# Performance work log

Hardware: AMD Instinct MI355X
Metric: run time of the kernel (lower is better)

The kernel has to match this reference:

```python
import jax, jax.numpy as jnp
import numpy as np

B = 128      # batch
U = 64       # num_users (H dim)
A = 64       # num_aps   (W dim)
FIN = 1      # input_feature_dim
FPHI = 32    # phi_feature_dim
FGAM = 32    # gamma_feature_dim
PHI_OUT = 2 * FPHI   # 64
GAM_OUT = 2 * FGAM   # 64


def setup_inputs() -> dict:
    key = jax.random.key(0)
    ks = iter(jax.random.split(key, 64))

    def w(shape, scale=0.05):
        return jax.random.normal(next(ks), shape, dtype=jnp.float32) * scale

    inp = {"channel_gains": jax.random.normal(next(ks), (B, FIN, U, A), dtype=jnp.float32)}
    # Phi1: conv1 (2*FIN -> 2*FPHI), conv2 (2*FPHI -> PHI_OUT)
    inp["phi1_W1"] = w((2 * FPHI, 2 * FIN)); inp["phi1_b1"] = w((2 * FPHI,))
    inp["phi1_W2"] = w((PHI_OUT, 2 * FPHI)); inp["phi1_b2"] = w((PHI_OUT,))
    # Phi2-5 (stacked): conv1 (GAM_OUT+FIN -> 2*FPHI), conv2 (2*FPHI -> PHI_OUT)
    inp["phiK_W1"] = w((4, 2 * FPHI, GAM_OUT + FIN)); inp["phiK_b1"] = w((4, 2 * FPHI))
    inp["phiK_W2"] = w((4, PHI_OUT, 2 * FPHI)); inp["phiK_b2"] = w((4, PHI_OUT))
    # Gamma1: conv1 (FIN+PHI_OUT -> 2*FGAM), conv2 (2*FGAM -> GAM_OUT)
    inp["gamma1_W1"] = w((2 * FGAM, FIN + PHI_OUT)); inp["gamma1_b1"] = w((2 * FGAM,))
    inp["gamma1_W2"] = w((GAM_OUT, 2 * FGAM)); inp["gamma1_b2"] = w((GAM_OUT,))
    # Gamma2-4 (stacked): conv1 (GAM_OUT+PHI_OUT -> 2*FGAM), conv2 (2*FGAM -> GAM_OUT)
    inp["gammaK_W1"] = w((3, 2 * FGAM, GAM_OUT + PHI_OUT)); inp["gammaK_b1"] = w((3, 2 * FGAM))
    inp["gammaK_W2"] = w((3, GAM_OUT, 2 * FGAM)); inp["gammaK_b2"] = w((3, GAM_OUT))
    # Gamma5 (final): conv1 (GAM_OUT+PHI_OUT -> 2*FGAM), conv2 (2*FGAM -> 1)
    inp["gamma5_W1"] = w((2 * FGAM, GAM_OUT + PHI_OUT)); inp["gamma5_b1"] = w((2 * FGAM,))
    inp["gamma5_W2"] = w((1, 2 * FGAM)); inp["gamma5_b2"] = w((1,))
    return inp


def conv1x1(x, W, b):
    # 1x1 conv on NCHW == per-pixel GEMM over channels
    return jnp.einsum('bcua,oc->boua', x, W) + b[None, :, None, None]


def post_users(x, f, ex_u):
    # keep first f channels; aggregate (sum-exclude-self over users) the next f
    c0 = x[:, :f]
    c1 = jnp.einsum('uv,bcva->bcua', ex_u, x[:, f:2 * f]) / (U - 1)
    return jnp.concatenate([c0, c1], axis=1)


def phi_block(x, W1, b1, W2, b2, ex_u):
    r = post_users(jax.nn.relu(conv1x1(x, W1, b1)), FPHI, ex_u)
    return post_users(conv1x1(r, W2, b2), FPHI, ex_u)


def gamma_block(x, W1, b1, W2, b2, ex_u, final):
    r = post_users(jax.nn.relu(conv1x1(x, W1, b1)), FGAM, ex_u)
    r = conv1x1(r, W2, b2)
    if not final:
        r = post_users(jax.nn.relu(r), FGAM, ex_u)
    return r


def reference(channel_gains, phi1_W1, phi1_b1, phi1_W2, phi1_b2,
              phiK_W1, phiK_b1, phiK_W2, phiK_b2,
              gamma1_W1, gamma1_b1, gamma1_W2, gamma1_b2,
              gammaK_W1, gammaK_b1, gammaK_W2, gammaK_b2,
              gamma5_W1, gamma5_b1, gamma5_W2, gamma5_b2):
    ex_u = jnp.ones((U, U), jnp.float32) - jnp.eye(U, dtype=jnp.float32)
    ex_a = jnp.ones((A, A), jnp.float32) - jnp.eye(A, dtype=jnp.float32)

    def node(msgs, feats, W1, b1, W2, b2, final):
        agg = jnp.einsum('bcuv,va->bcua', msgs, ex_a) / (A - 1)
        return gamma_block(jnp.concatenate([feats, agg], axis=1), W1, b1, W2, b2, ex_u, final)

    cg = channel_gains
    msgs = phi_block(jnp.concatenate([cg, cg], axis=1), phi1_W1, phi1_b1, phi1_W2, phi1_b2, ex_u)
    r = node(msgs, cg, gamma1_W1, gamma1_b1, gamma1_W2, gamma1_b2, False)
    for i in range(4):  # phi2..phi5 / gamma2..gamma5
        msgs = phi_block(jnp.concatenate([cg, r], axis=1),
                         phiK_W1[i], phiK_b1[i], phiK_W2[i], phiK_b2[i], ex_u)
        if i < 3:
            r = node(msgs, r, gammaK_W1[i], gammaK_b1[i], gammaK_W2[i], gammaK_b2[i], False)
        else:
            r = node(msgs, r, gamma5_W1, gamma5_b1, gamma5_W2, gamma5_b2, True)
    return r
```

## Files before the change

kernel.cpp:

```cpp
#include <hip/hip_runtime.h>


typedef __attribute__((ext_vector_type(8))) short bf16x8;
typedef __attribute__((ext_vector_type(4))) float f32x4;
typedef unsigned int u32;
typedef unsigned short u16;

__device__ __forceinline__ u32 bf16_rne(float x) {
    u32 u = __float_as_uint(x);
    return (u + 0x7fffu + ((u >> 16) & 1u)) >> 16;
}
__device__ __forceinline__ float bflo(u32 w) { return __uint_as_float(w << 16); }
__device__ __forceinline__ float bfhi(u32 w) { return __uint_as_float(w & 0xffff0000u); }

__device__ __forceinline__ u32 cvt2(float a, float b) {
    u32 w;
    asm("v_cvt_pk_bf16_f32 %0, %1, %2" : "=v"(w) : "v"(a), "v"(b));
    return w;
}

template <int CTRL>
__device__ __forceinline__ float dpp_mov(float v) {
    int x = __builtin_amdgcn_update_dpp(0, __float_as_int(v), CTRL, 0xF, 0xF, true);
    return __int_as_float(x);
}
__device__ __forceinline__ float row16_sum(float s) {
    s += dpp_mov<0xB1>(s);
    s += dpp_mov<0x4E>(s);
    s += dpp_mov<0x141>(s);
    s += dpp_mov<0x140>(s);
    return s;
}

__global__ __launch_bounds__(256) void prep_kernel(
    const float* __restrict__ cg, float* __restrict__ cgT,
    u16* __restrict__ packs, float* __restrict__ w0s,
    const float* __restrict__ phi1_W1, const float* __restrict__ phi1_W2,
    const float* __restrict__ phiK_W1, const float* __restrict__ phiK_W2,
    const float* __restrict__ g1_W1,   const float* __restrict__ g1_W2,
    const float* __restrict__ gK_W1,   const float* __restrict__ gK_W2,
    const float* __restrict__ g5_W1)
{
    const int bid = blockIdx.x;
    const int t = threadIdx.x;
    if (bid < 352) {
        int tid = bid * 256 + t;
        int layer, rem, nch;
        if (tid < 57344) { layer = tid >> 12; rem = tid & 4095; nch = 2; }
        else { layer = 14 + ((tid - 57344) >> 13); rem = (tid - 57344) & 8191; nch = 4; }
        const float* src; int stride, colOff; size_t dstBase;
        switch (layer) {
            case 0:  src = phi1_W2;                      stride = 64;  colOff = 0; dstBase = 0; break;
            case 1: case 2: case 3: case 4: {
                int k = layer - 1; src = phiK_W1 + k * 4160; stride = 65; colOff = 1;
                dstBase = 8192 + (size_t)k * 8192; break; }
            case 5: case 6: case 7: case 8: {
                int k = layer - 5; src = phiK_W2 + k * 4096; stride = 64; colOff = 0;
                dstBase = 40960 + (size_t)k * 8192; break; }
            case 9:  src = g1_W1;                        stride = 65;  colOff = 1; dstBase = 73728; break;
            case 10: src = g1_W2;                        stride = 64;  colOff = 0; dstBase = 81920; break;
            case 11: case 12: case 13: {
                int k = layer - 11; src = gK_W2 + k * 4096; stride = 64; colOff = 0;
                dstBase = 139264 + (size_t)k * 8192; break; }
            case 14: case 15: case 16: {
                int k = layer - 14; src = gK_W1 + k * 8192; stride = 128; colOff = 0;
                dstBase = 90112 + (size_t)k * 16384; break; }
            default: src = g5_W1;                        stride = 128; colOff = 0; dstBase = 163840; break;
        }
        int j = rem & 7;
        int lane = (rem >> 3) & 63;
        int rc = rem >> 9;
        int rb = rc / nch;
        int ch = rc - rb * nch;
        int o = 16 * rb + (lane & 15);
        int c = colOff + ch * 32 + (lane >> 4) * 8 + j;
        float wv = src[o * stride + c];
        u32 hb = bf16_rne(wv);
        u32 lb = bf16_rne(wv - bflo(hb));
        size_t base = dstBase + (size_t)rc * 1024 + lane * 8 + j;
        packs[base] = (u16)hb;
        packs[base + 512] = (u16)lb;
    } else if (bid < 354) {
        int i = (bid - 352) * 256 + t;
        if (i < 64)       w0s[i] = phi1_W1[i * 2] + phi1_W1[i * 2 + 1];
        else if (i < 320) { int k = (i - 64) >> 6; int o = (i - 64) & 63; w0s[i] = phiK_W1[k * 4160 + o * 65]; }
        else if (i < 384) { int o = i - 320; w0s[i] = g1_W1[o * 65]; }
    } else {
        int idx = (bid - 354) * 256 + t;
        int b = idx >> 12;
        int u = idx & 63;
        cgT[idx] = cg[((b << 6) + u) * 64 + ((idx >> 6) & 63)];
    }
}

template <int NCH, bool LO>
__device__ __forceinline__ void loadA(const u16* __restrict__ A, int lane, int wv,
                                      bf16x8* __restrict__ Ah, bf16x8* __restrict__ Al) {
#pragma unroll
    for (int ch = 0; ch < NCH; ++ch) {
        const u16* p = A + ((size_t)(wv * NCH + ch) * 2) * 512 + lane * 8;
        Ah[ch] = *(const bf16x8*)p;
        if constexpr (LO) Al[ch] = *(const bf16x8*)(p + 512);
    }
}

template <int NCH, int SROW, int CB, bool LO>
__device__ __forceinline__ void mfma_frags(const bf16x8* __restrict__ Ah,
                                           const bf16x8* __restrict__ Al,
                                           const u16* Xhi,
                                           int lane, f32x4 acc[4]) {
    const int n16 = lane & 15, q4 = lane >> 4;
#pragma unroll
    for (int ch = 0; ch < NCH; ++ch) {
#pragma unroll
        for (int tt = 0; tt < 4; ++tt) {
            int boff = (16 * tt + n16) * SROW + CB + ch * 32 + q4 * 8;
            bf16x8 Bh = *(const bf16x8*)(Xhi + boff);
            acc[tt] = __builtin_amdgcn_mfma_f32_16x16x32_bf16(Ah[ch], Bh, acc[tt], 0, 0, 0);
            if constexpr (LO)
                acc[tt] = __builtin_amdgcn_mfma_f32_16x16x32_bf16(Al[ch], Bh, acc[tt], 0, 0, 0);
        }
    }
}

__device__ __forceinline__ void post_users_regs(f32x4 acc[4], int wv) {
    constexpr float inv63 = 1.0f / 63.0f;
    if (wv >= 2) {
#pragma unroll
        for (int r = 0; r < 4; ++r) {
            float s = row16_sum(acc[0][r] + acc[1][r] + acc[2][r] + acc[3][r]) * inv63;
#pragma unroll
            for (int tt = 0; tt < 4; ++tt) acc[tt][r] = fmaf(acc[tt][r], -inv63, s);
        }
    }
}

template <int SROW, int CB>
__device__ __forceinline__ void stage_h(const f32x4 acc[4], u16* Xhi,
                                        int lane, int wv) {
    const int n16 = lane & 15, q4 = lane >> 4;
#pragma unroll
    for (int tt = 0; tt < 4; ++tt) {
        u32 h01 = cvt2(acc[tt][0], acc[tt][1]);
        u32 h23 = cvt2(acc[tt][2], acc[tt][3]);
        int off = (16 * tt + n16) * SROW + CB + 16 * wv + 4 * q4;
        *(uint2*)(Xhi + off) = make_uint2(h01, h23);
    }
}

template <int SROW, int CB>
__device__ __forceinline__ void stage_agg(const u32* __restrict__ ms,
                                          const float* __restrict__ Ss,
                                          u16* Xhi, int t) {
    constexpr float inv63 = 1.0f / 63.0f;
#pragma unroll
    for (int q = 0; q < 4; ++q) {
        int grp = q * 256 + t;
        int u = grp >> 4, c4 = (grp & 15) * 4;
        uint2 mw = *(const uint2*)(ms + u * 32 + (c4 >> 1));
        float4 sv = *(const float4*)(Ss + u * 64 + c4);
        float a0 = fmaf(bflo(mw.x), -inv63, sv.x);
        float a1 = fmaf(bfhi(mw.x), -inv63, sv.y);
        float a2 = fmaf(bflo(mw.y), -inv63, sv.z);
        float a3 = fmaf(bfhi(mw.y), -inv63, sv.w);
        int off = u * SROW + CB + c4;
        *(uint2*)(Xhi + off) = make_uint2(cvt2(a0, a1), cvt2(a2, a3));
    }
}

__global__ __launch_bounds__(256) void reduce_kernel(
    const u32* __restrict__ msgs, float* __restrict__ S)
{
    constexpr float inv63 = 1.0f / 63.0f;
    int idx = blockIdx.x * 256 + threadIdx.x;
    int b = idx >> 10;
    int j2 = idx & 1023;
    const u32* p = msgs + (size_t)b * 131072 + j2 * 2;
    float s0 = 0.0f, s1 = 0.0f, s2 = 0.0f, s3 = 0.0f;
#pragma unroll 8
    for (int a = 0; a < 64; ++a) {
        uint2 w = *(const uint2*)(p + (size_t)a * 2048);
        s0 += bflo(w.x);
        s1 += bfhi(w.x);
        s2 += bflo(w.y);
        s3 += bfhi(w.y);
    }
    float4 o = make_float4(s0 * inv63, s1 * inv63, s2 * inv63, s3 * inv63);
    *(float4*)(S + (size_t)b * 4096 + 4 * j2) = o;
}

__global__ __launch_bounds__(256) void phi1_kernel(
    const float* __restrict__ cgT,
    const float* __restrict__ w0, const float* __restrict__ b1,
    const u16* __restrict__ A2, const float* __restrict__ b2,
    u16* __restrict__ mOut)
{
    constexpr int SROW = 136;
    __shared__ __align__(16) u16 Xhi[64 * SROW];
    const int t = threadIdx.x;
    const u32 sb = blockIdx.x;
    const int lane = t & 63;
    const int wv = t >> 6;
    const int n16 = lane & 15, q4 = lane >> 4;

    bf16x8 A2h[2], A2l[2];
    loadA<2, false>(A2, lane, wv, A2h, A2l);

    f32x4 acc[4];
    {
        const float4 bv = *(const float4*)(b1 + 16 * wv + 4 * q4);
        const float4 w0v = *(const float4*)(w0 + 16 * wv + 4 * q4);
#pragma unroll
        for (int tt = 0; tt < 4; ++tt) {
            float cgv = cgT[(size_t)sb * 64 + 16 * tt + n16];
            acc[tt][0] = bv.x + w0v.x * cgv; acc[tt][1] = bv.y + w0v.y * cgv;
            acc[tt][2] = bv.z + w0v.z * cgv; acc[tt][3] = bv.w + w0v.w * cgv;
        }
    }
#pragma unroll
    for (int tt = 0; tt < 4; ++tt)
#pragma unroll
        for (int r = 0; r < 4; ++r) acc[tt][r] = fmaxf(acc[tt][r], 0.0f);
    post_users_regs(acc, wv);
    stage_h<SROW, 0>(acc, Xhi, lane, wv);
    __syncthreads();

    f32x4 acc2[4];
    {
        const float4 bv = *(const float4*)(b2 + 16 * wv + 4 * q4);
#pragma unroll
        for (int tt = 0; tt < 4; ++tt) { acc2[tt][0] = bv.x; acc2[tt][1] = bv.y; acc2[tt][2] = bv.z; acc2[tt][3] = bv.w; }
    }
    mfma_frags<2, SROW, 0, false>(A2h, A2l, Xhi, lane, acc2);
    post_users_regs(acc2, wv);
    stage_h<SROW, 64>(acc2, Xhi, lane, wv);
    __syncthreads();
    u16* oM = mOut + (size_t)sb * 4096;
#pragma unroll
    for (int q = 0; q < 2; ++q) {
        int grp = q * 256 + t;
        int u = grp >> 3, c8 = (grp & 7) * 8;
        *(uint4*)(oM + u * 64 + c8) = *(const uint4*)(Xhi + u * SROW + 64 + c8);
    }
}

template <int KG, bool LO>
__global__ __launch_bounds__(256) void fused_kernel(
    const float* __restrict__ cgT,
    const u16* __restrict__ rIn,
    const u32* __restrict__ mIn, const float* __restrict__ Sin,
    const u16* __restrict__ A1g, const float* __restrict__ w0g,
    const float* __restrict__ b1g,
    const u16* __restrict__ A2g, const float* __restrict__ b2g,
    const u16* __restrict__ A1p, const float* __restrict__ w0p,
    const float* __restrict__ b1p,
    const u16* __restrict__ A2p, const float* __restrict__ b2p,
    u16* __restrict__ rOut, u16* __restrict__ mOut)
{
    constexpr int SROW = (KG == 128 && LO) ? 200 : 136;
    constexpr int HB   = (SROW == 200) ? 128 : 64;
    __shared__ __align__(16) u16 Xhi[64 * SROW];
    const int t = threadIdx.x;
    const u32 sb = blockIdx.x;
    const u32 bloc = sb >> 6;
    const int lane = t & 63;
    const int wv = t >> 6;
    const int n16 = lane & 15, q4 = lane >> 4;
    constexpr int NCH1 = KG / 32;

    bf16x8 A1h[NCH1], A1l[NCH1];
    loadA<NCH1, LO>(A1g, lane, wv, A1h, A1l);

    float cgvv[4];
#pragma unroll
    for (int tt = 0; tt < 4; ++tt) cgvv[tt] = cgT[(size_t)sb * 64 + 16 * tt + n16];

    if constexpr (KG == 128) {
        const u16* rs = rIn + (size_t)sb * 4096;
#pragma unroll
        for (int q = 0; q < 2; ++q) {
            int grp = q * 256 + t;
            int u = grp >> 3, c8 = (grp & 7) * 8;
            *(uint4*)(Xhi + u * SROW + c8) = *(const uint4*)(rs + u * 64 + c8);
        }
    }
    stage_agg<SROW, KG - 64>(mIn + (size_t)sb * 2048, Sin + (size_t)bloc * 4096,
                             Xhi, t);
    __syncthreads();

    bf16x8 A2h[2], A2l[2];
    loadA<2, LO>(A2g, lane, wv, A2h, A2l);

    f32x4 acc[4];
    {
        const float4 bv = *(const float4*)(b1g + 16 * wv + 4 * q4);
#pragma unroll
        for (int tt = 0; tt < 4; ++tt) { acc[tt][0] = bv.x; acc[tt][1] = bv.y; acc[tt][2] = bv.z; acc[tt][3] = bv.w; }
    }
    if constexpr (KG == 64) {
        const float4 w0v = *(const float4*)(w0g + 16 * wv + 4 * q4);
#pragma unroll
        for (int tt = 0; tt < 4; ++tt) {
            acc[tt][0] += w0v.x * cgvv[tt]; acc[tt][1] += w0v.y * cgvv[tt];
            acc[tt][2] += w0v.z * cgvv[tt]; acc[tt][3] += w0v.w * cgvv[tt];
        }
    }
    mfma_frags<NCH1, SROW, 0, LO>(A1h, A1l, Xhi, lane, acc);
#pragma unroll
    for (int tt = 0; tt < 4; ++tt)
#pragma unroll
        for (int r = 0; r < 4; ++r) acc[tt][r] = fmaxf(acc[tt][r], 0.0f);
    post_users_regs(acc, wv);
    if constexpr (HB < KG) __syncthreads();
    stage_h<SROW, HB>(acc, Xhi, lane, wv);
    __syncthreads();

    bf16x8 A3h[2], A3l[2];
    loadA<2, LO>(A1p, lane, wv, A3h, A3l);

    f32x4 acc2[4];
    {
        const float4 bv = *(const float4*)(b2g + 16 * wv + 4 * q4);
#pragma unroll
        for (int tt = 0; tt < 4; ++tt) { acc2[tt][0] = bv.x; acc2[tt][1] = bv.y; acc2[tt][2] = bv.z; acc2[tt][3] = bv.w; }
    }
    mfma_frags<2, SROW, HB, LO>(A2h, A2l, Xhi, lane, acc2);
#pragma unroll
    for (int tt = 0; tt < 4; ++tt)
#pragma unroll
        for (int r = 0; r < 4; ++r) acc2[tt][r] = fmaxf(acc2[tt][r], 0.0f);
    post_users_regs(acc2, wv);
    stage_h<SROW, 0>(acc2, Xhi, lane, wv);
    __syncthreads();

    {
        u16* oH = rOut + (size_t)sb * 4096;
#pragma unroll
        for (int q = 0; q < 2; ++q) {
            int grp = q * 256 + t;
            int u = grp >> 3, c8 = (grp & 7) * 8;
            *(uint4*)(oH + u * 64 + c8) = *(const uint4*)(Xhi + u * SROW + c8);
        }
    }
    bf16x8 A4h[2], A4l[2];
    loadA<2, LO>(A2p, lane, wv, A4h, A4l);

    f32x4 acc3[4];
    {
        const float4 bv = *(const float4*)(b1p + 16 * wv + 4 * q4);
        const float4 w0v = *(const float4*)(w0p + 16 * wv + 4 * q4);
#pragma unroll
        for (int tt = 0; tt < 4; ++tt) {
            acc3[tt][0] = bv.x + w0v.x * cgvv[tt]; acc3[tt][1] = bv.y + w0v.y * cgvv[tt];
            acc3[tt][2] = bv.z + w0v.z * cgvv[tt]; acc3[tt][3] = bv.w + w0v.w * cgvv[tt];
        }
    }
    mfma_frags<2, SROW, 0, LO>(A3h, A3l, Xhi, lane, acc3);
#pragma unroll
    for (int tt = 0; tt < 4; ++tt)
#pragma unroll
        for (int r = 0; r < 4; ++r) acc3[tt][r] = fmaxf(acc3[tt][r], 0.0f);
    post_users_regs(acc3, wv);
    stage_h<SROW, HB>(acc3, Xhi, lane, wv);
    __syncthreads();

    f32x4 acc4[4];
    {
        const float4 bv = *(const float4*)(b2p + 16 * wv + 4 * q4);
#pragma unroll
        for (int tt = 0; tt < 4; ++tt) { acc4[tt][0] = bv.x; acc4[tt][1] = bv.y; acc4[tt][2] = bv.z; acc4[tt][3] = bv.w; }
    }
    mfma_frags<2, SROW, HB, LO>(A4h, A4l, Xhi, lane, acc4);
    post_users_regs(acc4, wv);
    stage_h<SROW, 0>(acc4, Xhi, lane, wv);
    __syncthreads();
    u16* oM = mOut + (size_t)sb * 4096;
#pragma unroll
    for (int q = 0; q < 2; ++q) {
        int grp = q * 256 + t;
        int u = grp >> 3, c8 = (grp & 7) * 8;
        *(uint4*)(oM + u * 64 + c8) = *(const uint4*)(Xhi + u * SROW + c8);
    }
}

__global__ __launch_bounds__(256) void final_kernel(
    const u16* __restrict__ rIn,
    const u32* __restrict__ mIn, const float* __restrict__ Sin,
    const u16* __restrict__ A1, const float* __restrict__ b1,
    const float* __restrict__ w2raw, const float* __restrict__ b2raw,
    float* __restrict__ outF)
{
    constexpr int SROW = 136;
    __shared__ __align__(16) u16 Xhi[64 * SROW];
    __shared__ float part[4][64];
    const int t = threadIdx.x;
    const u32 sb = blockIdx.x;
    const u32 bloc = sb >> 6;
    const int lane = t & 63;
    const int wv = t >> 6;
    const int q4 = lane >> 4;

    bf16x8 A1h[4], A1l[4];
    loadA<4, true>(A1, lane, wv, A1h, A1l);

    {
        const u16* rs = rIn + (size_t)sb * 4096;
#pragma unroll
        for (int q = 0; q < 2; ++q) {
            int grp = q * 256 + t;
            int u = grp >> 3, c8 = (grp & 7) * 8;
            *(uint4*)(Xhi + u * SROW + c8) = *(const uint4*)(rs + u * 64 + c8);
        }
    }
    stage_agg<SROW, 64>(mIn + (size_t)sb * 2048, Sin + (size_t)bloc * 4096,
                        Xhi, t);
    __syncthreads();

    f32x4 acc[4];
    {
        const float4 bv = *(const float4*)(b1 + 16 * wv + 4 * q4);
#pragma unroll
        for (int tt = 0; tt < 4; ++tt) { acc[tt][0] = bv.x; acc[tt][1] = bv.y; acc[tt][2] = bv.z; acc[tt][3] = bv.w; }
    }
    mfma_frags<4, SROW, 0, true>(A1h, A1l, Xhi, lane, acc);
#pragma unroll
    for (int tt = 0; tt < 4; ++tt)
#pragma unroll
        for (int r = 0; r < 4; ++r) acc[tt][r] = fmaxf(acc[tt][r], 0.0f);
    post_users_regs(acc, wv);
    __syncthreads();
    stage_h<SROW, 64>(acc, Xhi, lane, wv);

    const int cb2 = 16 * wv;
    const u16* hr = Xhi + lane * SROW + 64 + cb2;
    bf16x8 h0 = *(const bf16x8*)hr;
    bf16x8 h1 = *(const bf16x8*)(hr + 8);
    float sum = 0.0f;
#pragma unroll
    for (int j = 0; j < 8; ++j) {
        sum += w2raw[cb2 + j] * bflo((u32)(u16)h0[j]);
        sum += w2raw[cb2 + 8 + j] * bflo((u32)(u16)h1[j]);
    }
    part[wv][lane] = sum;
    __syncthreads();
    if (t < 64) {
        float o = b2raw[0] + part[0][t] + part[1][t] + part[2][t] + part[3][t];
        outF[((size_t)bloc * 64 + t) * 64 + (sb & 63)] = o;
    }
}

extern "C" void kernel_launch(void* const* d_in, const int* in_sizes, int n_in,
                              void* d_out, int out_size, void* d_ws, size_t ws_size,
                              hipStream_t stream) {
    const float* cg      = (const float*)d_in[0];
    const float* phi1_W1 = (const float*)d_in[1];
    const float* phi1_b1 = (const float*)d_in[2];
    const float* phi1_W2 = (const float*)d_in[3];
    const float* phi1_b2 = (const float*)d_in[4];
    const float* phiK_W1 = (const float*)d_in[5];
    const float* phiK_b1 = (const float*)d_in[6];
    const float* phiK_W2 = (const float*)d_in[7];
    const float* phiK_b2 = (const float*)d_in[8];
    const float* g1_W1   = (const float*)d_in[9];
    const float* g1_b1   = (const float*)d_in[10];
    const float* g1_W2   = (const float*)d_in[11];
    const float* g1_b2   = (const float*)d_in[12];
    const float* gK_W1   = (const float*)d_in[13];
    const float* gK_b1   = (const float*)d_in[14];
    const float* gK_W2   = (const float*)d_in[15];
    const float* gK_b2   = (const float*)d_in[16];
    const float* g5_W1   = (const float*)d_in[17];
    const float* g5_b1   = (const float*)d_in[18];
    const float* g5_W2   = (const float*)d_in[19];
    const float* g5_b2   = (const float*)d_in[20];
    (void)in_sizes; (void)n_in; (void)out_size;

    int BC = 128;
    while (BC > 4 && (size_t)BC * 1064960 + 2461696 > ws_size) BC >>= 1;
    const int NC = 128 / BC;

    u16*   rHi  = (u16*)d_ws;
    u16*   msgs = rHi + (size_t)BC * 262144;
    float* S    = (float*)(msgs + (size_t)BC * 262144);
    float* cgT  = S + (size_t)BC * 4096;
    u16*   Apack = (u16*)(cgT + 524288);
    float* w0s  = (float*)(Apack + 180224);
    float* out  = (float*)d_out;

    prep_kernel<<<354 + 2048, 256, 0, stream>>>(cg, cgT, Apack, w0s,
        phi1_W1, phi1_W2, phiK_W1, phiK_W2, g1_W1, g1_W2, gK_W1, gK_W2, g5_W1);

    const int nblk = BC * 64;
    const int rblk = BC * 4;

    for (int c = 0; c < NC; ++c) {
        const float* cgTc = cgT + (size_t)c * BC * 4096;
        float* outc = out + (size_t)c * BC * 4096;

        phi1_kernel<<<nblk, 256, 0, stream>>>(cgTc, w0s, phi1_b1,
            Apack + 0, phi1_b2, msgs);
        reduce_kernel<<<rblk, 256, 0, stream>>>((const u32*)msgs, S);

        fused_kernel<64, false><<<nblk, 256, 0, stream>>>(cgTc, nullptr,
            (const u32*)msgs, S,
            Apack + 73728, w0s + 320, g1_b1, Apack + 81920, g1_b2,
            Apack + 8192, w0s + 64, phiK_b1, Apack + 40960, phiK_b2,
            rHi, msgs);
        reduce_kernel<<<rblk, 256, 0, stream>>>((const u32*)msgs, S);

        for (int j = 0; j < 3; ++j) {
            auto kern = (j < 2) ? fused_kernel<128, false> : fused_kernel<128, true>;
            kern<<<nblk, 256, 0, stream>>>(cgTc, rHi,
                (const u32*)msgs, S,
                Apack + 90112 + (size_t)j * 16384, nullptr, gK_b1 + j * 64,
                Apack + 139264 + (size_t)j * 8192, gK_b2 + j * 64,
                Apack + 8192 + (size_t)(j + 1) * 8192, w0s + 64 + (j + 1) * 64,
                phiK_b1 + (j + 1) * 64,
                Apack + 40960 + (size_t)(j + 1) * 8192, phiK_b2 + (j + 1) * 64,
                rHi, msgs);
            reduce_kernel<<<rblk, 256, 0, stream>>>((const u32*)msgs, S);
        }

        final_kernel<<<nblk, 256, 0, stream>>>(rHi, (const u32*)msgs, S,
            Apack + 163840, g5_b1, g5_W2, g5_b2, outc);
    }
}
```

Baseline: 413.1 us.

## Process two super-blocks per workgroup in fused kernel to amortize weight loads

Each fused_kernel workgroup now handles two super-blocks (blockIdx and blockIdx+gridDim) with a doubled LDS buffer, and the grid is halved. Weight fragments loaded into registers are reused across both, and the two independent MFMA chains can interleave to hide latency. In exchange, LDS use and register pressure roughly double, which lowers occupancy and halves the number of workgroups.

```diff
diff --git a/kernel.cpp b/kernel.cpp
--- a/kernel.cpp
+++ b/kernel.cpp
@@ -259,127 +259,146 @@
 {
     constexpr int SROW = (KG == 128 && LO) ? 200 : 136;
     constexpr int HB   = (SROW == 200) ? 128 : 64;
-    __shared__ __align__(16) u16 Xhi[64 * SROW];
+    __shared__ __align__(16) u16 Xhi[2][64 * SROW];
     const int t = threadIdx.x;
-    const u32 sb = blockIdx.x;
-    const u32 bloc = sb >> 6;
     const int lane = t & 63;
     const int wv = t >> 6;
     const int n16 = lane & 15, q4 = lane >> 4;
     constexpr int NCH1 = KG / 32;
 
+    const u32 sb0 = blockIdx.x;
+    const u32 sb1 = blockIdx.x + gridDim.x;
+
     bf16x8 A1h[NCH1], A1l[NCH1];
     loadA<NCH1, LO>(A1g, lane, wv, A1h, A1l);
 
-    float cgvv[4];
-#pragma unroll
-    for (int tt = 0; tt < 4; ++tt) cgvv[tt] = cgT[(size_t)sb * 64 + 16 * tt + n16];
-
-    if constexpr (KG == 128) {
-        const u16* rs = rIn + (size_t)sb * 4096;
+    float cgvv[2][4];
+#pragma unroll
+    for (int tt = 0; tt < 4; ++tt) {
+        cgvv[0][tt] = cgT[(size_t)sb0 * 64 + 16 * tt + n16];
+        cgvv[1][tt] = cgT[(size_t)sb1 * 64 + 16 * tt + n16];
+    }
+
+#pragma unroll
+    for (int s = 0; s < 2; ++s) {
+        const u32 sb = s ? sb1 : sb0;
+        if constexpr (KG == 128) {
+            const u16* rs = rIn + (size_t)sb * 4096;
+#pragma unroll
+            for (int q = 0; q < 2; ++q) {
+                int grp = q * 256 + t;
+                int u = grp >> 3, c8 = (grp & 7) * 8;
+                *(uint4*)(&Xhi[s][u * SROW + c8]) = *(const uint4*)(rs + u * 64 + c8);
+            }
+        }
+        stage_agg<SROW, KG - 64>(mIn + (size_t)sb * 2048,
+                                 Sin + (size_t)(sb >> 6) * 4096, Xhi[s], t);
+    }
+    __syncthreads();
+
+    bf16x8 A2h[2], A2l[2];
+    loadA<2, LO>(A2g, lane, wv, A2h, A2l);
+
+    f32x4 acc[2][4];
+#pragma unroll
+    for (int s = 0; s < 2; ++s) {
+        const float4 bv = *(const float4*)(b1g + 16 * wv + 4 * q4);
+#pragma unroll
+        for (int tt = 0; tt < 4; ++tt) { acc[s][tt][0] = bv.x; acc[s][tt][1] = bv.y; acc[s][tt][2] = bv.z; acc[s][tt][3] = bv.w; }
+        if constexpr (KG == 64) {
+            const float4 w0v = *(const float4*)(w0g + 16 * wv + 4 * q4);
+#pragma unroll
+            for (int tt = 0; tt < 4; ++tt) {
+                acc[s][tt][0] += w0v.x * cgvv[s][tt]; acc[s][tt][1] += w0v.y * cgvv[s][tt];
+                acc[s][tt][2] += w0v.z * cgvv[s][tt]; acc[s][tt][3] += w0v.w * cgvv[s][tt];
+            }
+        }
+        mfma_frags<NCH1, SROW, 0, LO>(A1h, A1l, Xhi[s], lane, acc[s]);
+#pragma unroll
+        for (int tt = 0; tt < 4; ++tt)
+#pragma unroll
+            for (int r = 0; r < 4; ++r) acc[s][tt][r] = fmaxf(acc[s][tt][r], 0.0f);
+        post_users_regs(acc[s], wv);
+    }
+    if constexpr (HB < KG) __syncthreads();
+#pragma unroll
+    for (int s = 0; s < 2; ++s) stage_h<SROW, HB>(acc[s], Xhi[s], lane, wv);
+    __syncthreads();
+
+    bf16x8 A3h[2], A3l[2];
+    loadA<2, LO>(A1p, lane, wv, A3h, A3l);
+
+    f32x4 acc2[2][4];
+#pragma unroll
+    for (int s = 0; s < 2; ++s) {
+        const float4 bv = *(const float4*)(b2g + 16 * wv + 4 * q4);
+#pragma unroll
+        for (int tt = 0; tt < 4; ++tt) { acc2[s][tt][0] = bv.x; acc2[s][tt][1] = bv.y; acc2[s][tt][2] = bv.z; acc2[s][tt][3] = bv.w; }
+        mfma_frags<2, SROW, HB, LO>(A2h, A2l, Xhi[s], lane, acc2[s]);
+#pragma unroll
+        for (int tt = 0; tt < 4; ++tt)
+#pragma unroll
+            for (int r = 0; r < 4; ++r) acc2[s][tt][r] = fmaxf(acc2[s][tt][r], 0.0f);
+        post_users_regs(acc2[s], wv);
+        stage_h<SROW, 0>(acc2[s], Xhi[s], lane, wv);
+    }
+    __syncthreads();
+
+#pragma unroll
+    for (int s = 0; s < 2; ++s) {
+        u16* oH = rOut + (size_t)(s ? sb1 : sb0) * 4096;
 #pragma unroll
         for (int q = 0; q < 2; ++q) {
             int grp = q * 256 + t;
             int u = grp >> 3, c8 = (grp & 7) * 8;
-            *(uint4*)(Xhi + u * SROW + c8) = *(const uint4*)(rs + u * 64 + c8);
-        }
-    }
-    stage_agg<SROW, KG - 64>(mIn + (size_t)sb * 2048, Sin + (size_t)bloc * 4096,
-                             Xhi, t);
-    __syncthreads();
-
-    bf16x8 A2h[2], A2l[2];
-    loadA<2, LO>(A2g, lane, wv, A2h, A2l);
-
-    f32x4 acc[4];
-    {
-        const float4 bv = *(const float4*)(b1g + 16 * wv + 4 * q4);
-#pragma unroll
-        for (int tt = 0; tt < 4; ++tt) { acc[tt][0] = bv.x; acc[tt][1] = bv.y; acc[tt][2] = bv.z; acc[tt][3] = bv.w; }
-    }
-    if constexpr (KG == 64) {
-        const float4 w0v = *(const float4*)(w0g + 16 * wv + 4 * q4);
+            *(uint4*)(oH + u * 64 + c8) = *(const uint4*)(&Xhi[s][u * SROW + c8]);
+        }
+    }
+    bf16x8 A4h[2], A4l[2];
+    loadA<2, LO>(A2p, lane, wv, A4h, A4l);
+
+    f32x4 acc3[2][4];
+#pragma unroll
+    for (int s = 0; s < 2; ++s) {
+        const float4 bv = *(const float4*)(b1p + 16 * wv + 4 * q4);
+        const float4 w0v = *(const float4*)(w0p + 16 * wv + 4 * q4);
 #pragma unroll
         for (int tt = 0; tt < 4; ++tt) {
-            acc[tt][0] += w0v.x * cgvv[tt]; acc[tt][1] += w0v.y * cgvv[tt];
-            acc[tt][2] += w0v.z * cgvv[tt]; acc[tt][3] += w0v.w * cgvv[tt];
-        }
-    }
-    mfma_frags<NCH1, SROW, 0, LO>(A1h, A1l, Xhi, lane, acc);
-#pragma unroll
-    for (int tt = 0; tt < 4; ++tt)
-#pragma unroll
-        for (int r = 0; r < 4; ++r) acc[tt][r] = fmaxf(acc[tt][r], 0.0f);
-    post_users_regs(acc, wv);
-    if constexpr (HB < KG) __syncthreads();
-    stage_h<SROW, HB>(acc, Xhi, lane, wv);
-    __syncthreads();
-
-    bf16x8 A3h[2], A3l[2];
-    loadA<2, LO>(A1p, lane, wv, A3h, A3l);
-
-    f32x4 acc2[4];
-    {
-        const float4 bv = *(const float4*)(b2g + 16 * wv + 4 * q4);
-#pragma unroll
-        for (int tt = 0; tt < 4; ++tt) { acc2[tt][0] = bv.x; acc2[tt][1] = bv.y; acc2[tt][2] = bv.z; acc2[tt][3] = bv.w; }
-    }
-    mfma_frags<2, SROW, HB, LO>(A2h, A2l, Xhi, lane, acc2);
-#pragma unroll
-    for (int tt = 0; tt < 4; ++tt)
-#pragma unroll
-        for (int r = 0; r < 4; ++r) acc2[tt][r] = fmaxf(acc2[tt][r], 0.0f);
-    post_users_regs(acc2, wv);
-    stage_h<SROW, 0>(acc2, Xhi, lane, wv);
-    __syncthreads();
-
-    {
-        u16* oH = rOut + (size_t)sb * 4096;
+            acc3[s][tt][0] = bv.x + w0v.x * cgvv[s][tt];
+            acc3[s][tt][1] = bv.y + w0v.y * cgvv[s][tt];
+            acc3[s][tt][2] = bv.z + w0v.z * cgvv[s][tt];
+            acc3[s][tt][3] = bv.w + w0v.w * cgvv[s][tt];
+        }
+        mfma_frags<2, SROW, 0, LO>(A3h, A3l, Xhi[s], lane, acc3[s]);
+#pragma unroll
+        for (int tt = 0; tt < 4; ++tt)
+#pragma unroll
+            for (int r = 0; r < 4; ++r) acc3[s][tt][r] = fmaxf(acc3[s][tt][r], 0.0f);
+        post_users_regs(acc3[s], wv);
+        stage_h<SROW, HB>(acc3[s], Xhi[s], lane, wv);
+    }
+    __syncthreads();
+
+    f32x4 acc4[2][4];
+#pragma unroll
+    for (int s = 0; s < 2; ++s) {
+        const float4 bv = *(const float4*)(b2p + 16 * wv + 4 * q4);
+#pragma unroll
+        for (int tt = 0; tt < 4; ++tt) { acc4[s][tt][0] = bv.x; acc4[s][tt][1] = bv.y; acc4[s][tt][2] = bv.z; acc4[s][tt][3] = bv.w; }
+        mfma_frags<2, SROW, HB, LO>(A4h, A4l, Xhi[s], lane, acc4[s]);
+        post_users_regs(acc4[s], wv);
+        stage_h<SROW, 0>(acc4[s], Xhi[s], lane, wv);
+    }
+    __syncthreads();
+#pragma unroll
+    for (int s = 0; s < 2; ++s) {
+        u16* oM = mOut + (size_t)(s ? sb1 : sb0) * 4096;
 #pragma unroll
         for (int q = 0; q < 2; ++q) {
             int grp = q * 256 + t;
             int u = grp >> 3, c8 = (grp & 7) * 8;
-            *(uint4*)(oH + u * 64 + c8) = *(const uint4*)(Xhi + u * SROW + c8);
-        }
-    }
-    bf16x8 A4h[2], A4l[2];
-    loadA<2, LO>(A2p, lane, wv, A4h, A4l);
-
-    f32x4 acc3[4];
-    {
-        const float4 bv = *(const float4*)(b1p + 16 * wv + 4 * q4);
-        const float4 w0v = *(const float4*)(w0p + 16 * wv + 4 * q4);
-#pragma unroll
-        for (int tt = 0; tt < 4; ++tt) {
-            acc3[tt][0] = bv.x + w0v.x * cgvv[tt]; acc3[tt][1] = bv.y + w0v.y * cgvv[tt];
-            acc3[tt][2] = bv.z + w0v.z * cgvv[tt]; acc3[tt][3] = bv.w + w0v.w * cgvv[tt];
-        }
-    }
-    mfma_frags<2, SROW, 0, LO>(A3h, A3l, Xhi, lane, acc3);
-#pragma unroll
-    for (int tt = 0; tt < 4; ++tt)
-#pragma unroll
-        for (int r = 0; r < 4; ++r) acc3[tt][r] = fmaxf(acc3[tt][r], 0.0f);
-    post_users_regs(acc3, wv);
-    stage_h<SROW, HB>(acc3, Xhi, lane, wv);
-    __syncthreads();
-
-    f32x4 acc4[4];
-    {
-        const float4 bv = *(const float4*)(b2p + 16 * wv + 4 * q4);
-#pragma unroll
-        for (int tt = 0; tt < 4; ++tt) { acc4[tt][0] = bv.x; acc4[tt][1] = bv.y; acc4[tt][2] = bv.z; acc4[tt][3] = bv.w; }
-    }
-    mfma_frags<2, SROW, HB, LO>(A4h, A4l, Xhi, lane, acc4);
-    post_users_regs(acc4, wv);
-    stage_h<SROW, 0>(acc4, Xhi, lane, wv);
-    __syncthreads();
-    u16* oM = mOut + (size_t)sb * 4096;
-#pragma unroll
-    for (int q = 0; q < 2; ++q) {
-        int grp = q * 256 + t;
-        int u = grp >> 3, c8 = (grp & 7) * 8;
-        *(uint4*)(oM + u * 64 + c8) = *(const uint4*)(Xhi + u * SROW + c8);
+            *(uint4*)(oM + u * 64 + c8) = *(const uint4*)(&Xhi[s][u * SROW + c8]);
+        }
     }
 }
 
@@ -501,7 +520,7 @@
             Apack + 0, phi1_b2, msgs);
         reduce_kernel<<<rblk, 256, 0, stream>>>((const u32*)msgs, S);
 
-        fused_kernel<64, false><<<nblk, 256, 0, stream>>>(cgTc, nullptr,
+        fused_kernel<64, false><<<nblk / 2, 256, 0, stream>>>(cgTc, nullptr,
             (const u32*)msgs, S,
             Apack + 73728, w0s + 320, g1_b1, Apack + 81920, g1_b2,
             Apack + 8192, w0s + 64, phiK_b1, Apack + 40960, phiK_b2,
@@ -510,7 +529,7 @@
 
         for (int j = 0; j < 3; ++j) {
             auto kern = (j < 2) ? fused_kernel<128, false> : fused_kernel<128, true>;
-            kern<<<nblk, 256, 0, stream>>>(cgTc, rHi,
+            kern<<<nblk / 2, 256, 0, stream>>>(cgTc, rHi,
                 (const u32*)msgs, S,
                 Apack + 90112 + (size_t)j * 16384, nullptr, gK_b1 + j * 64,
                 Apack + 139264 + (size_t)j * 8192, gK_b2 + j * 64,
```

After: 417.8 us. Within noise of the previous version (+1.1%).
